# Kernel tuning notes

Hardware: AMD Instinct MI355X
Metric: run time of the kernel (lower is better)

## Reference

```python
import jax, jax.numpy as jnp
import numpy as np

SIGMA = 1.0
DELTA = 1.0
TOPK = 10
TOPK_HALF = 5  # int(np.around(TOPK / 2))


def l2norm(x):
    # F.normalize: x / max(||x||, 1e-12)
    n = jnp.linalg.norm(x, axis=-1, keepdims=True)
    return x / jnp.maximum(n, 1e-12)


def cdist(a, b):
    # pairwise euclidean distance with grad-safe sqrt (0 on exact-zero dists)
    d2 = (jnp.sum(a * a, axis=1)[:, None] + jnp.sum(b * b, axis=1)[None, :]
          - 2.0 * a @ b.T)
    d2 = jnp.maximum(d2, 0.0)
    return jnp.where(d2 > 0.0, jnp.sqrt(jnp.where(d2 > 0.0, d2, 1.0)), 0.0)


def rc_weights(t_emb, idx):
    # all of this is under torch.no_grad() in the original
    N = t_emb.shape[0]
    T_dist = cdist(t_emb, t_emb)
    W_P = jnp.exp(-(T_dist ** 2) / SIGMA)
    same_id = idx[:, None] == idx[None, :]
    W_P_copy = jnp.where(same_id, 1.0, W_P)
    _, topk_index = jax.lax.top_k(W_P_copy, TOPK)            # [N, k]
    topk_half_index = topk_index[:, :TOPK_HALF]               # [N, k/2]
    rows = jnp.arange(N)[:, None]
    W_NN = jnp.zeros((N, N), W_P.dtype).at[rows, topk_index].set(1.0)
    V = (((W_NN + W_NN.T) / 2.0) == 1.0).astype(W_P.dtype)    # mutual-NN graph
    # vectorized form of the per-row loop:
    # W_C_tilda[i, j] = V[i, j] * |N(i) \cap N(j)| / |N(i)|
    deg = V.sum(axis=1)                                       # |N(i)| per row
    VV = V @ V                                                # V symmetric -> (V@V)[i,j] = |N(i) cap N(j)|
    W_C_tilda = jnp.where(V > 0.0, VV / jnp.maximum(deg, 1.0)[:, None], 0.0)
    W_C_hat = W_C_tilda[topk_half_index].mean(axis=1)         # [N, N]
    W_C = (W_C_hat + W_C_hat.T) / 2.0
    W = (W_P + W_C) / 2.0
    off_diag = 1.0 - jnp.eye(N, dtype=W.dtype)
    pos_weight = W * off_diag
    neg_weight = (1.0 - W) * off_diag
    return pos_weight, neg_weight


def rc_loss(s_emb, t_emb, idx):
    s_emb = l2norm(s_emb)        # disable_mu=True
    t_emb = l2norm(t_emb)
    N = s_emb.shape[0]
    S_dist = cdist(s_emb, s_emb)
    S_dist = S_dist / S_dist.mean(axis=1, keepdims=True)
    pos_w, neg_w = rc_weights(t_emb, idx)
    pos_w = jax.lax.stop_gradient(pos_w)
    neg_w = jax.lax.stop_gradient(neg_w)
    pull = jax.nn.relu(S_dist) ** 2 * pos_w
    push = jax.nn.relu(DELTA - S_dist) ** 2 * neg_w
    return (pull.sum() + push.sum()) / (N * (N - 1))


def kl_loss(s_f, s_g):
    # disable_mu=True -> normalize both
    s_f = l2norm(s_f)
    s_g = l2norm(s_g)
    N = s_f.shape[0]
    S_dist = cdist(s_f, s_f)
    S_dist = S_dist / S_dist.mean(axis=1, keepdims=True)
    S_bg = cdist(s_g, s_g)
    S_bg = S_bg / S_bg.mean(axis=1, keepdims=True)
    log_q = jax.nn.log_softmax(-S_dist, axis=-1)
    log_p = jax.nn.log_softmax(jax.lax.stop_gradient(-S_bg), axis=-1)
    p = jnp.exp(log_p)
    return jnp.sum(p * (log_p - log_q)) / N


def setup_inputs() -> dict:
    key = jax.random.key(0)
    k1, k2, k3, k4 = jax.random.split(key, 4)
    N = 4096
    s_f = jax.random.normal(k1, (N, 512), jnp.float32)
    s_g = jax.random.normal(k2, (N, 512), jnp.float32)
    t_g = jax.random.normal(k3, (N, 1024), jnp.float32)
    idx = jax.random.randint(k4, (N,), 0, 2048, jnp.int64 if jax.config.jax_enable_x64 else jnp.int32)
    return {"s_f": s_f, "s_g": s_g, "t_g": t_g, "idx": idx}


def reference(s_f, s_g, t_g, idx):
    loss_RC_f = rc_loss(s_f, t_g, idx)
    loss_RC_g = rc_loss(s_g, t_g, idx)
    loss_RC = (loss_RC_f + loss_RC_g) / 2.0
    loss_KL = kl_loss(s_f, s_g)
    return loss_RC, loss_KL, loss_RC + loss_KL
```

## Files before the change

### kernel.cpp

```cpp
#include <hip/hip_runtime.h>
#include <hip/hip_bf16.h>

#define NN 4096
typedef unsigned short u16;
typedef __bf16 bf16x8 __attribute__((ext_vector_type(8)));
typedef float f32x4 __attribute__((ext_vector_type(4)));
typedef u16 u16x8 __attribute__((ext_vector_type(8)));

typedef const __attribute__((address_space(1))) void* gptr_t;
typedef __attribute__((address_space(3))) void* lptr_t;

__device__ inline u16 bf16bits(float v) {
    __bf16 h = (__bf16)v;
    return __builtin_bit_cast(u16, h);
}
__device__ inline float bf16val(float v) {
    __bf16 h = (__bf16)v;
    return (float)h;
}
__device__ inline float b2f(u16 b) { return __uint_as_float(((unsigned)b) << 16); }

__device__ inline float block_sum(float v, volatile float* sbuf) {
    int lane = threadIdx.x & 63, wv = threadIdx.x >> 6;
#pragma unroll
    for (int o = 32; o > 0; o >>= 1) v += __shfl_xor(v, o, 64);
    if (lane == 0) sbuf[wv] = v;
    __syncthreads();
    float r = sbuf[0] + sbuf[1] + sbuf[2] + sbuf[3];
    __syncthreads();
    return r;
}

template <int D>
__global__ void normalize_kernel(const float* __restrict__ in, u16* __restrict__ outb,
                                 float* __restrict__ ssout) {
    __shared__ float sbuf[4];
    constexpr int NV = D / 4;
    int row = blockIdx.x, tid = threadIdx.x;
    const float4* x4 = (const float4*)(in + (size_t)row * D);
    float4 v = make_float4(0.f, 0.f, 0.f, 0.f);
    if (tid < NV) v = x4[tid];
    float s = v.x * v.x + v.y * v.y + v.z * v.z + v.w * v.w;
    float tot = block_sum(s, sbuf);
    float inv = 1.0f / fmaxf(sqrtf(tot), 1e-12f);
    float sb = 0.f;
    if (tid < NV) {
        float b0 = bf16val(v.x * inv), b1 = bf16val(v.y * inv);
        float b2 = bf16val(v.z * inv), b3 = bf16val(v.w * inv);
        ushort4 o;
        o.x = bf16bits(v.x * inv);
        o.y = bf16bits(v.y * inv);
        o.z = bf16bits(v.z * inv);
        o.w = bf16bits(v.w * inv);
        ((ushort4*)(outb + (size_t)row * D))[tid] = o;
        sb = b0 * b0 + b1 * b1 + b2 * b2 + b3 * b3;
    }
    float totb = block_sum(sb, sbuf);
    if (tid == 0) ssout[row] = totb;
}

#define TS 132
__launch_bounds__(256)
__global__ void gram_merged(const u16* __restrict__ tb, const u16* __restrict__ fb,
                            const u16* __restrict__ gb, const float* __restrict__ ss_t,
                            const float* __restrict__ ss_f, const float* __restrict__ ss_g,
                            u16* __restrict__ WP, u16* __restrict__ Sf, u16* __restrict__ Sg) {
    __shared__ __align__(16) u16 smem[24576];

    int bid = blockIdx.x;
    int seg = (bid < 528) ? 0 : (bid < 1056 ? 1 : 2);
    int p = bid - seg * 528;
    int l = (p & 7) * 66 + (p >> 3);
    int by = 0, rem = l;
    while (rem >= 32 - by) { rem -= 32 - by; ++by; }
    int bx = by + rem;

    const u16* X = (seg == 0) ? tb : (seg == 1 ? fb : gb);
    const float* ss = (seg == 0) ? ss_t : (seg == 1 ? ss_f : ss_g);
    u16* outp = (seg == 0) ? WP : (seg == 1 ? Sf : Sg);
    const int K = (seg == 0) ? 1024 : 512;
    const bool mode1 = (seg != 0);
    const bool offdiag = (bx != by);

    const int tid = threadIdx.x;
    const int wv = tid >> 6, lane = tid & 63;
    const int wr = wv >> 1, wc = wv & 1;
    const int brow = by * 128, bcol = bx * 128;
    const int r = lane & 15, kc = lane >> 4;
    const int crow = lane >> 2;
    const int koff = (lane & 3) * 8;

    f32x4 acc[4][4];
#pragma unroll
    for (int mi = 0; mi < 4; ++mi)
#pragma unroll
        for (int ni = 0; ni < 4; ++ni) acc[mi][ni] = (f32x4){0.f, 0.f, 0.f, 0.f};

    auto STAGE = [&](int buf, int k0) {
#pragma unroll
        for (int cc = 0; cc < 2; ++cc) {
            int c = wv * 2 + cc;
            const u16* ga = X + (size_t)(brow + c * 16 + crow) * K + k0 + koff;
            const u16* gbp = X + (size_t)(bcol + c * 16 + crow) * K + k0 + koff;
            __builtin_amdgcn_global_load_lds((gptr_t)ga, (lptr_t)&smem[buf * 4096 + c * 512], 16, 0, 0);
            __builtin_amdgcn_global_load_lds((gptr_t)gbp, (lptr_t)&smem[12288 + buf * 4096 + c * 512], 16, 0, 0);
        }
    };

    const int NT = K / 32;
    STAGE(0, 0);
    STAGE(1, 32);
    for (int t = 0; t < NT; ++t) {
        int cur = t % 3;
        if (t == NT - 1) asm volatile("s_waitcnt vmcnt(0)" ::: "memory");
        else             asm volatile("s_waitcnt vmcnt(4)" ::: "memory");
        __builtin_amdgcn_sched_barrier(0);
        __builtin_amdgcn_s_barrier();
        __builtin_amdgcn_sched_barrier(0);

        bf16x8 af[4], bfr[4];
#pragma unroll
        for (int mi = 0; mi < 4; ++mi)
            af[mi] = *(const bf16x8*)&smem[cur * 4096 + (wr * 64 + mi * 16 + r) * 32 + kc * 8];
#pragma unroll
        for (int ni = 0; ni < 4; ++ni)
            bfr[ni] = *(const bf16x8*)&smem[12288 + cur * 4096 + (wc * 64 + ni * 16 + r) * 32 + kc * 8];

        if (t + 2 < NT) STAGE((t + 2) % 3, (t + 2) * 32);

        asm volatile("s_waitcnt lgkmcnt(0)" ::: "memory");
        __builtin_amdgcn_sched_barrier(0);

#pragma unroll
        for (int mi = 0; mi < 4; ++mi)
#pragma unroll
            for (int ni = 0; ni < 4; ++ni)
                acc[mi][ni] = __builtin_amdgcn_mfma_f32_16x16x32_bf16(af[mi], bfr[ni], acc[mi][ni], 0, 0, 0);
    }
    __syncthreads();

    u16* tile = smem;
    const int q = lane >> 4;
#pragma unroll
    for (int mi = 0; mi < 4; ++mi) {
#pragma unroll
        for (int v = 0; v < 4; ++v) {
            int rl = wr * 64 + mi * 16 + q * 4 + v;
            float ssi = ss[brow + rl];
#pragma unroll
            for (int ni = 0; ni < 4; ++ni) {
                int cl = wc * 64 + ni * 16 + r;
                float d2 = fmaxf(ssi + ss[bcol + cl] - 2.0f * acc[mi][ni][v], 0.f);
                float o = mode1 ? sqrtf(d2) : __expf(-d2);
                tile[rl * TS + cl] = bf16bits(o);
            }
        }
    }
    __syncthreads();

    {
        int rl = tid >> 1, hf = tid & 1;
        const u16* srow = &tile[rl * TS + hf * 64];
        u16* drow = outp + (size_t)(brow + rl) * NN + bcol + hf * 64;
#pragma unroll
        for (int i = 0; i < 8; ++i) {
            ushort4 aa = *(const ushort4*)(srow + i * 8);
            ushort4 bb = *(const ushort4*)(srow + i * 8 + 4);
            u16x8 pk = {aa.x, aa.y, aa.z, aa.w, bb.x, bb.y, bb.z, bb.w};
            *(u16x8*)(drow + i * 8) = pk;
        }
    }

    if (offdiag) {
        int c = tid >> 1, hf = tid & 1;
        u16* drow = outp + (size_t)(bcol + c) * NN + brow + hf * 64;
#pragma unroll
        for (int s = 0; s < 8; ++s) {
            u16 g[8];
#pragma unroll
            for (int u = 0; u < 8; ++u) g[u] = tile[(hf * 64 + s * 8 + u) * TS + c];
            u16x8 pk = {g[0], g[1], g[2], g[3], g[4], g[5], g[6], g[7]};
            *(u16x8*)(drow + s * 8) = pk;
        }
    }
}

__global__ void topk_kernel(const u16* __restrict__ WP, const int* __restrict__ idx,
                            int* __restrict__ topk) {
    __shared__ unsigned long long wlist[4][10];
    int row = blockIdx.x, tid = threadIdx.x;
    int lane = tid & 63, wv = tid >> 6;
    int myid = idx[row];
    const u16x8* W8 = (const u16x8*)(WP + (size_t)row * NN);
    const int4* idx4 = (const int4*)idx;
    unsigned key[16];
#pragma unroll
    for (int a = 0; a < 2; ++a) {
        u16x8 w = W8[a * 256 + tid];
        int4 iA = idx4[a * 512 + tid * 2];
        int4 iB = idx4[a * 512 + tid * 2 + 1];
        int ids[8] = {iA.x, iA.y, iA.z, iA.w, iB.x, iB.y, iB.z, iB.w};
#pragma unroll
        for (int c = 0; c < 8; ++c)
            key[a * 8 + c] = (ids[c] == myid) ? 0x3F800000u : (((unsigned)w[c]) << 16);
    }
    for (int it = 0; it < 10; ++it) {
        unsigned long long best = 0;
#pragma unroll
        for (int a = 0; a < 2; ++a)
#pragma unroll
            for (int c = 0; c < 8; ++c) {
                unsigned j = (unsigned)(a * 2048 + tid * 8 + c);
                unsigned long long pk =
                    ((unsigned long long)key[a * 8 + c] << 32) | (0xFFFFFFFFu - j);
                if (pk > best) best = pk;
            }
#pragma unroll
        for (int o = 32; o > 0; o >>= 1) {
            unsigned long long t = __shfl_xor(best, o, 64);
            if (t > best) best = t;
        }
        if (lane == 0) wlist[wv][it] = best;
        unsigned jstar = 0xFFFFFFFFu - (unsigned)(best & 0xFFFFFFFFu);
        if (((jstar >> 3) & 255u) == (unsigned)tid) {
            unsigned slot = ((jstar >> 11) << 3) | (jstar & 7u);
#pragma unroll
            for (int a = 0; a < 16; ++a)
                if ((unsigned)a == slot) key[a] = 0u;
        }
    }
    __syncthreads();
    if (tid == 0) {
        int h0 = 0, h1 = 0, h2 = 0, h3 = 0;
        for (int it = 0; it < 10; ++it) {
            unsigned long long c0 = wlist[0][h0], c1 = wlist[1][h1];
            unsigned long long c2 = wlist[2][h2], c3 = wlist[3][h3];
            unsigned long long m01 = c0 > c1 ? c0 : c1;
            unsigned long long m23 = c2 > c3 ? c2 : c3;
            unsigned long long m = m01 > m23 ? m01 : m23;
            if (m == c0) ++h0;
            else if (m == c1) ++h1;
            else if (m == c2) ++h2;
            else ++h3;
            topk[row * 10 + it] = (int)(0xFFFFFFFFu - (unsigned)(m & 0xFFFFFFFFu));
        }
    }
}

__global__ void mutual_kernel(const int* __restrict__ topk, int* __restrict__ nbr,
                              int* __restrict__ deg) {
    int gid = blockIdx.x * 256 + threadIdx.x;
    if (gid >= NN * 10) return;
    int i = gid / 10, a = gid - i * 10;
    int j = topk[i * 10 + a];
    bool mut = false;
#pragma unroll
    for (int b = 0; b < 10; ++b) mut = mut || (topk[j * 10 + b] == i);
    nbr[gid] = mut ? j : -1;
    if (mut) atomicAdd(&deg[i], 1);
}

__global__ void tilda_kernel(const int* __restrict__ nbr, const int* __restrict__ deg,
                             float* __restrict__ tvals) {
    int gid = blockIdx.x * 256 + threadIdx.x;
    if (gid >= NN * 10) return;
    int m = gid / 10;
    int j = nbr[gid];
    if (j < 0) { tvals[gid] = 0.f; return; }
    int am[10], aj[10];
#pragma unroll
    for (int p = 0; p < 10; ++p) am[p] = nbr[m * 10 + p];
#pragma unroll
    for (int p = 0; p < 10; ++p) aj[p] = nbr[j * 10 + p];
    int cnt = 0;
#pragma unroll
    for (int p = 0; p < 10; ++p)
#pragma unroll
        for (int qq = 0; qq < 10; ++qq)
            cnt += (am[p] >= 0 && am[p] == aj[qq]) ? 1 : 0;
    int dm = deg[m];
    float dv = (float)(dm > 1 ? dm : 1);
    tvals[gid] = (float)cnt / dv;
}

__global__ void hat_kernel(const int* __restrict__ topk, const int* __restrict__ nbr,
                           const float* __restrict__ tvals, int* __restrict__ hcols,
                           float* __restrict__ hvals) {
    int gid = blockIdx.x * 256 + threadIdx.x;
    if (gid >= NN * 5) return;
    int i = gid / 5, h = gid - i * 5;
    int m = topk[i * 10 + h];
#pragma unroll
    for (int a = 0; a < 10; ++a) {
        int j = nbr[m * 10 + a];
        int slot = i * 50 + h * 10 + a;
        hcols[slot] = j;
        hvals[slot] = (j >= 0) ? tvals[m * 10 + a] * 0.2f : 0.f;
    }
}

__global__ void fused_dense_kernel(const u16* __restrict__ Sf, const u16* __restrict__ Sg,
                                   const u16* __restrict__ WP, float* __restrict__ rsf,
                                   float* __restrict__ rsg, double* __restrict__ acc) {
    __shared__ float sbuf[4];
    int row = blockIdx.x, tid = threadIdx.x;
    const u16x8* f8 = (const u16x8*)(Sf + (size_t)row * NN);
    const u16x8* g8 = (const u16x8*)(Sg + (size_t)row * NN);
    const u16x8* w8 = (const u16x8*)(WP + (size_t)row * NN);
    u16x8 fr[2], gr[2], wr2[2];
#pragma unroll
    for (int a = 0; a < 2; ++a) {
        fr[a] = f8[a * 256 + tid];
        gr[a] = g8[a * 256 + tid];
        wr2[a] = w8[a * 256 + tid];
    }
    float sf_ = 0.f, sg_ = 0.f;
#pragma unroll
    for (int a = 0; a < 2; ++a)
#pragma unroll
        for (int c = 0; c < 8; ++c) {
            sf_ += b2f(fr[a][c]);
            sg_ += b2f(gr[a][c]);
        }
    float rsum_f = block_sum(sf_, sbuf);
    float rsum_g = block_sum(sg_, sbuf);
    if (tid == 0) {
        rsf[row] = rsum_f;
        rsg[row] = rsum_g;
    }
    float imf = (float)NN / rsum_f;
    float img = (float)NN / rsum_g;
    float vf[16], vg[16];
#pragma unroll
    for (int a = 0; a < 2; ++a)
#pragma unroll
        for (int c = 0; c < 8; ++c) {
            vf[a * 8 + c] = b2f(fr[a][c]) * imf;
            vg[a * 8 + c] = b2f(gr[a][c]) * img;
        }
    float ef = 0.f, eg = 0.f;
#pragma unroll
    for (int a = 0; a < 16; ++a) {
        ef += __expf(-vf[a]);
        eg += __expf(-vg[a]);
    }
    float lf = logf(block_sum(ef, sbuf));
    float lg = logf(block_sum(eg, sbuf));
    float af = 0.f, ag = 0.f, akl = 0.f;
#pragma unroll
    for (int a = 0; a < 2; ++a) {
#pragma unroll
        for (int c = 0; c < 8; ++c) {
            int j = a * 2048 + tid * 8 + c;
            float wp = b2f(wr2[a][c]);
            float sf = vf[a * 8 + c], sg = vg[a * 8 + c];
            if (j != row) {
                float t = fmaxf(1.f - sf, 0.f);
                float pu = t * t;
                float gq = sf * sf - pu;
                af += pu + 0.5f * gq * wp;
                t = fmaxf(1.f - sg, 0.f);
                pu = t * t;
                gq = sg * sg - pu;
                ag += pu + 0.5f * gq * wp;
            }
            float lq = -sf - lf;
            float lp = -sg - lg;
            float pp = __expf(lp);
            akl += pp * (lp - lq);
        }
    }
    float tf = block_sum(af, sbuf);
    float tg2 = block_sum(ag, sbuf);
    float tk = block_sum(akl, sbuf);
    if (tid == 0) {
        int bank = (row & 63) * 8;
        atomicAdd(&acc[bank + 0], (double)tf);
        atomicAdd(&acc[bank + 1], (double)tg2);
        atomicAdd(&acc[bank + 2], (double)tk);
    }
}

__global__ void sparse_kernel(const u16* __restrict__ Sf, const u16* __restrict__ Sg,
                              const int* __restrict__ hcols, const float* __restrict__ hvals,
                              const float* __restrict__ rsf, const float* __restrict__ rsg,
                              double* __restrict__ acc) {
    __shared__ float sbuf[4];
    int lane = threadIdx.x & 63, wv = threadIdx.x >> 6;
    int i = blockIdx.x * 4 + wv;
    float cf = 0.f, cg = 0.f;
    if (lane < 50) {
        int j = hcols[i * 50 + lane];
        if (j >= 0 && j != i) {
            float v = hvals[i * 50 + lane];
            float imfi = (float)NN / rsf[i];
            float imgi = (float)NN / rsg[i];
            float s1 = b2f(Sf[(size_t)i * NN + j]) * imfi;
            float s2 = b2f(Sf[(size_t)j * NN + i]) * ((float)NN / rsf[j]);
            float t1 = fmaxf(1.f - s1, 0.f), t2 = fmaxf(1.f - s2, 0.f);
            cf = v * ((s1 * s1 - t1 * t1) + (s2 * s2 - t2 * t2));
            s1 = b2f(Sg[(size_t)i * NN + j]) * imgi;
            s2 = b2f(Sg[(size_t)j * NN + i]) * ((float)NN / rsg[j]);
            t1 = fmaxf(1.f - s1, 0.f);
            t2 = fmaxf(1.f - s2, 0.f);
            cg = v * ((s1 * s1 - t1 * t1) + (s2 * s2 - t2 * t2));
        }
    }
    float tf = block_sum(cf, sbuf);
    float tg = block_sum(cg, sbuf);
    if (threadIdx.x == 0) {
        int bank = (blockIdx.x & 63) * 8;
        atomicAdd(&acc[bank + 0], (double)(0.25f * tf));
        atomicAdd(&acc[bank + 1], (double)(0.25f * tg));
    }
}

__global__ void finalize_kernel(const double* __restrict__ acc, float* __restrict__ out) {
    if (threadIdx.x == 0) {
        double a0 = 0.0, a1 = 0.0, a2 = 0.0;
        for (int b = 0; b < 64; ++b) {
            a0 += acc[b * 8 + 0];
            a1 += acc[b * 8 + 1];
            a2 += acc[b * 8 + 2];
        }
        double denom = (double)NN * (double)(NN - 1);
        double rcf = a0 / denom, rcg = a1 / denom;
        double rc = 0.5 * (rcf + rcg);
        double kl = a2 / (double)NN;
        out[0] = (float)rc;
        out[1] = (float)kl;
        out[2] = (float)(rc + kl);
    }
}

extern "C" void kernel_launch(void* const* d_in, const int* in_sizes, int n_in, void* d_out,
                              int out_size, void* d_ws, size_t ws_size, hipStream_t stream) {
    const float* s_f = (const float*)d_in[0];
    const float* s_g = (const float*)d_in[1];
    const float* t_g = (const float*)d_in[2];
    const int* idx = (const int*)d_in[3];
    float* out = (float*)d_out;

    char* base = (char*)d_ws;
    size_t off = 0;
    auto alloc = [&](size_t b) {
        char* p = base + off;
        off = (off + b + 255) & ~(size_t)255;
        return p;
    };
    double* acc = (double*)alloc(64 * 8 * 8);
    int* deg = (int*)alloc(NN * 4);
    size_t zero_bytes = off;
    float* rowsum_f = (float*)alloc(NN * 4);
    float* rowsum_g = (float*)alloc(NN * 4);
    u16* tb = (u16*)alloc((size_t)NN * 1024 * 2);
    u16* fb = (u16*)alloc((size_t)NN * 512 * 2);
    u16* gb = (u16*)alloc((size_t)NN * 512 * 2);
    float* ss_t = (float*)alloc(NN * 4);
    float* ss_f = (float*)alloc(NN * 4);
    float* ss_g = (float*)alloc(NN * 4);
    u16* WP = (u16*)alloc((size_t)NN * NN * 2);
    u16* Sf = (u16*)alloc((size_t)NN * NN * 2);
    u16* Sg = (u16*)alloc((size_t)NN * NN * 2);
    int* topk = (int*)alloc(NN * 10 * 4);
    int* nbr = (int*)alloc(NN * 10 * 4);
    float* tvals = (float*)alloc(NN * 10 * 4);
    int* hcols = (int*)alloc(NN * 50 * 4);
    float* hvals = (float*)alloc(NN * 50 * 4);

    hipMemsetAsync(d_ws, 0, zero_bytes, stream);

    normalize_kernel<1024><<<NN, 256, 0, stream>>>(t_g, tb, ss_t);
    normalize_kernel<512><<<NN, 256, 0, stream>>>(s_f, fb, ss_f);
    normalize_kernel<512><<<NN, 256, 0, stream>>>(s_g, gb, ss_g);

    gram_merged<<<1584, 256, 0, stream>>>(tb, fb, gb, ss_t, ss_f, ss_g, WP, Sf, Sg);

    topk_kernel<<<NN, 256, 0, stream>>>(WP, idx, topk);
    mutual_kernel<<<(NN * 10 + 255) / 256, 256, 0, stream>>>(topk, nbr, deg);
    tilda_kernel<<<(NN * 10 + 255) / 256, 256, 0, stream>>>(nbr, deg, tvals);
    hat_kernel<<<(NN * 5 + 255) / 256, 256, 0, stream>>>(topk, nbr, tvals, hcols, hvals);

    fused_dense_kernel<<<NN, 256, 0, stream>>>(Sf, Sg, WP, rowsum_f, rowsum_g, acc);
    sparse_kernel<<<NN / 4, 256, 0, stream>>>(Sf, Sg, hcols, hvals, rowsum_f, rowsum_g, acc);
    finalize_kernel<<<1, 64, 0, stream>>>(acc, out);
}
```

Baseline: 197.0 us.

## Give each wave private LDS staging to drop block barriers in gram loop

Each wave now loads its own 64-row A and B slices into a private double-buffered LDS region instead of sharing block-wide triple-buffered tiles. This removes the per-iteration s_barrier, since waves no longer read data staged by other waves. In exchange every operand tile is loaded twice (A rows shared by two waves, B rows by two waves), doubling global-to-LDS traffic. LDS per block grows to 64KB, which may reduce occupancy, and prefetch depth drops from two stages to one.

```diff
diff --git a/kernel.cpp b/kernel.cpp
--- a/kernel.cpp
+++ b/kernel.cpp
@@ -65,7 +65,7 @@
                             const u16* __restrict__ gb, const float* __restrict__ ss_t,
                             const float* __restrict__ ss_f, const float* __restrict__ ss_g,
                             u16* __restrict__ WP, u16* __restrict__ Sf, u16* __restrict__ Sg) {
-    __shared__ __align__(16) u16 smem[24576];
+    __shared__ __align__(16) u16 smem[32768];
 
     int bid = blockIdx.x;
     int seg = (bid < 528) ? 0 : (bid < 1056 ? 1 : 2);
@@ -89,6 +89,7 @@
     const int r = lane & 15, kc = lane >> 4;
     const int crow = lane >> 2;
     const int koff = (lane & 3) * 8;
+    const int wbase = wv * 8192;
 
     f32x4 acc[4][4];
 #pragma unroll
@@ -97,36 +98,36 @@
         for (int ni = 0; ni < 4; ++ni) acc[mi][ni] = (f32x4){0.f, 0.f, 0.f, 0.f};
 
     auto STAGE = [&](int buf, int k0) {
-#pragma unroll
-        for (int cc = 0; cc < 2; ++cc) {
-            int c = wv * 2 + cc;
-            const u16* ga = X + (size_t)(brow + c * 16 + crow) * K + k0 + koff;
-            const u16* gbp = X + (size_t)(bcol + c * 16 + crow) * K + k0 + koff;
-            __builtin_amdgcn_global_load_lds((gptr_t)ga, (lptr_t)&smem[buf * 4096 + c * 512], 16, 0, 0);
-            __builtin_amdgcn_global_load_lds((gptr_t)gbp, (lptr_t)&smem[12288 + buf * 4096 + c * 512], 16, 0, 0);
+        int wb = wbase + buf * 4096;
+#pragma unroll
+        for (int cc = 0; cc < 4; ++cc) {
+            const u16* ga = X + (size_t)(brow + wr * 64 + cc * 16 + crow) * K + k0 + koff;
+            const u16* gbp = X + (size_t)(bcol + wc * 64 + cc * 16 + crow) * K + k0 + koff;
+            __builtin_amdgcn_global_load_lds((gptr_t)ga, (lptr_t)&smem[wb + cc * 512], 16, 0, 0);
+            __builtin_amdgcn_global_load_lds((gptr_t)gbp, (lptr_t)&smem[wb + 2048 + cc * 512], 16, 0, 0);
         }
     };
 
     const int NT = K / 32;
     STAGE(0, 0);
-    STAGE(1, 32);
     for (int t = 0; t < NT; ++t) {
-        int cur = t % 3;
-        if (t == NT - 1) asm volatile("s_waitcnt vmcnt(0)" ::: "memory");
-        else             asm volatile("s_waitcnt vmcnt(4)" ::: "memory");
+        int cur = t & 1;
+        if (t + 1 < NT) {
+            STAGE(cur ^ 1, (t + 1) * 32);
+            asm volatile("s_waitcnt vmcnt(8)" ::: "memory");
+        } else {
+            asm volatile("s_waitcnt vmcnt(0)" ::: "memory");
+        }
         __builtin_amdgcn_sched_barrier(0);
-        __builtin_amdgcn_s_barrier();
-        __builtin_amdgcn_sched_barrier(0);
-
+
+        int wb = wbase + cur * 4096;
         bf16x8 af[4], bfr[4];
 #pragma unroll
         for (int mi = 0; mi < 4; ++mi)
-            af[mi] = *(const bf16x8*)&smem[cur * 4096 + (wr * 64 + mi * 16 + r) * 32 + kc * 8];
+            af[mi] = *(const bf16x8*)&smem[wb + (mi * 16 + r) * 32 + kc * 8];
 #pragma unroll
         for (int ni = 0; ni < 4; ++ni)
-            bfr[ni] = *(const bf16x8*)&smem[12288 + cur * 4096 + (wc * 64 + ni * 16 + r) * 32 + kc * 8];
-
-        if (t + 2 < NT) STAGE((t + 2) % 3, (t + 2) * 32);
+            bfr[ni] = *(const bf16x8*)&smem[wb + 2048 + (ni * 16 + r) * 32 + kc * 8];
 
         asm volatile("s_waitcnt lgkmcnt(0)" ::: "memory");
         __builtin_amdgcn_sched_barrier(0);
```

Measured after the change: 212.3 us. 1.08x slower.
